# Kernel optimization log

Measured on AMD Instinct MI355X. Metric: run time of the kernel, lower is better.

Reference implementation:

```python
import jax, jax.numpy as jnp
import numpy as np

EPS = 1e-5

def _conv(x, w, groups=1):
    # x: NCHW, w: OIHW, VALID padding, stride 1
    return jax.lax.conv_general_dilated(
        x, w, window_strides=(1, 1), padding='VALID',
        feature_group_count=groups,
        dimension_numbers=('NCHW', 'OIHW', 'NCHW'))

def _bn(x, gamma, beta, mean, var):
    # eval-mode BatchNorm2d over channel dim
    inv = jax.lax.rsqrt(var + EPS) * gamma
    return x * inv[None, :, None, None] + (beta - mean * inv)[None, :, None, None]

def _xcorr_depthwise(x, kernel):
    # per-sample depthwise cross-correlation via grouped conv
    B, C, H, W = x.shape
    xr = x.reshape(1, B * C, H, W)
    kr = kernel.reshape(B * C, 1, kernel.shape[2], kernel.shape[3])
    out = _conv(xr, kr, groups=B * C)  # [1, B*C, Ho, Wo]
    return out.reshape(B, C, out.shape[2], out.shape[3])

def setup_inputs() -> dict:
    key = jax.random.key(0)
    ks = jax.random.split(key, 16)
    B, Cin, H, Oc = 128, 256, 256, 256
    inp = {
        'kernel': jax.random.normal(ks[0], (B, Cin, 7, 7), jnp.float32),
        'search': jax.random.normal(ks[1], (B, Cin, 31, 31), jnp.float32),
        # conv_kernel tower
        'wk': jax.random.normal(ks[2], (H, Cin, 3, 3), jnp.float32) * 0.05,
        'gk': jax.random.normal(ks[3], (H,), jnp.float32) * 0.1 + 1.0,
        'bk': jax.random.normal(ks[4], (H,), jnp.float32) * 0.1,
        'mk': jax.random.normal(ks[5], (H,), jnp.float32) * 0.1,
        'vk': jax.random.uniform(ks[6], (H,), jnp.float32) + 0.5,
        # conv_search tower
        'ws': jax.random.normal(ks[7], (H, Cin, 3, 3), jnp.float32) * 0.05,
        'gs': jax.random.normal(ks[8], (H,), jnp.float32) * 0.1 + 1.0,
        'bs': jax.random.normal(ks[9], (H,), jnp.float32) * 0.1,
        'ms': jax.random.normal(ks[10], (H,), jnp.float32) * 0.1,
        'vs': jax.random.uniform(ks[11], (H,), jnp.float32) + 0.5,
        # head: 1x1 conv -> BN -> ReLU -> 1x1 conv (with bias)
        'wh1': jax.random.normal(ks[12], (H, H, 1, 1), jnp.float32) * 0.05,
        'gh': jax.random.normal(ks[13], (H,), jnp.float32) * 0.1 + 1.0,
        'bh': jax.random.normal(ks[14], (H,), jnp.float32) * 0.1,
        'mh': jnp.zeros((H,), jnp.float32),
        'vh': jnp.ones((H,), jnp.float32),
        'wh2': jax.random.normal(ks[15], (Oc, H, 1, 1), jnp.float32) * 0.05,
        'bh2': jnp.zeros((Oc,), jnp.float32),
    }
    return inp

def reference(kernel, search, wk, gk, bk, mk, vk, ws, gs, bs, ms, vs,
              wh1, gh, bh, mh, vh, wh2, bh2):
    k = jax.nn.relu(_bn(_conv(kernel, wk), gk, bk, mk, vk))   # [B,H,5,5]
    s = jax.nn.relu(_bn(_conv(search, ws), gs, bs, ms, vs))   # [B,H,29,29]
    feat = _xcorr_depthwise(s, k)                              # [B,H,25,25]
    h = jax.nn.relu(_bn(_conv(feat, wh1), gh, bh, mh, vh))
    out = _conv(h, wh2) + bh2[None, :, None, None]            # [B,Oc,25,25]
    return out
```

## Files before the change

### kernel.cpp

```cpp
#include <hip/hip_runtime.h>
#include <hip/hip_bf16.h>
#include <cstdint>
#include <cstddef>

typedef unsigned short u16;
typedef __attribute__((ext_vector_type(8))) __bf16 bf16x8;
typedef __attribute__((ext_vector_type(4))) float f32x4;

#define EPS_BN 1e-5f

__device__ __forceinline__ u16 f2bf(float f) {
    union { float f; uint32_t u; } v; v.f = f;
    uint32_t u = v.u;
    u += 0x7FFFu + ((u >> 16) & 1u);
    return (u16)(u >> 16);
}
__device__ __forceinline__ float bf2f(u16 s) {
    union { uint32_t u; float f; } v; v.u = ((uint32_t)s) << 16;
    return v.f;
}

union Pack8 { u16 u[8]; uint4 v4; };
union Pack4 { u16 u[4]; uint2 v2; };

typedef __attribute__((address_space(1))) const unsigned char as1c;
typedef __attribute__((address_space(3))) unsigned char as3;
__device__ __forceinline__ void gld_lds16(const void* g, void* l) {
    __builtin_amdgcn_global_load_lds((as1c*)g, (as3*)l, 16, 0, 0);
}

__device__ __forceinline__ void tr_tile(const float* __restrict__ in,
                                        u16* __restrict__ out,
                                        int P, int b, int p0)
{
    const int w  = threadIdx.x >> 6;
    const int ln = threadIdx.x & 63;
    const int p  = p0 + ln;
    const bool ok = (p < P);
    const int pc = ok ? p : (P - 1);
    const float* ib = in + ((size_t)b * 256 + w * 64) * P + pc;

    float v[64];
    #pragma unroll
    for (int i = 0; i < 64; i++)
        v[i] = ib[(size_t)i * P];

    if (ok) {
        u16* ob = out + ((size_t)(b * P + p)) * 256 + w * 64;
        #pragma unroll
        for (int k = 0; k < 8; k++) {
            Pack8 pk;
            #pragma unroll
            for (int i = 0; i < 8; i++)
                pk.u[i] = f2bf(v[k * 8 + i]);
            *(uint4*)(ob + k * 8) = pk.v4;
        }
    }
}

__global__ __launch_bounds__(256)
void tr_all(const float* __restrict__ s, const float* __restrict__ k,
            u16* __restrict__ so, u16* __restrict__ ko)
{
    int blk = blockIdx.x;
    if (blk < 2048) {
        tr_tile(s, so, 961, blk >> 4, (blk & 15) * 64);
    } else {
        tr_tile(k, ko, 49, blk - 2048, 0);
    }
}

template<int TAPS, bool NHWC_OUT, typename OutT, bool RELU>
__global__ __launch_bounds__(256)
void conv_gemm(const u16* __restrict__ in, const u16* __restrict__ W,
               const float* __restrict__ scale, const float* __restrict__ shift,
               OutT* __restrict__ out, int Hi, int Wi, int Ho, int Wo)
{
    constexpr int KT = TAPS * 256;
    constexpr int KB = KT / 64;
    const int HoWo = Ho * Wo;

    __shared__ u16 Alds[8192];
    __shared__ u16 Blds[8192];

    const int tid = threadIdx.x;
    const int it = blockIdx.x;
    const int jt = blockIdx.y;
    const int wv = tid >> 6;
    const int lane = tid & 63;

    const int c8 = tid & 7;
    const int t3 = tid >> 3;
    const int csw = c8 ^ (t3 & 7);

    const u16* gA[4];
    const u16* gB[4];
    #pragma unroll
    for (int q = 0; q < 4; q++) {
        int r = q * 32 + t3;
        gA[q] = W + (size_t)(it * 128 + r) * KT + csw * 8;
        int jg = jt * 128 + r;
        int bb = jg / HoWo;
        int msp = jg - bb * HoWo;
        int oyp = msp / Wo;
        int oxp = msp - oyp * Wo;
        gB[q] = in + ((size_t)(bb * Hi + oyp) * Wi + oxp) * 256 + csw * 8;
    }

    const int wi = (wv >> 1) * 64;
    const int wj = (wv & 1) * 64;
    const int lr = lane & 15;
    const int lq = lane >> 4;

    f32x4 acc[4][4];
    #pragma unroll
    for (int a = 0; a < 4; a++)
        #pragma unroll
        for (int b = 0; b < 4; b++)
            acc[a][b] = (f32x4){0.f, 0.f, 0.f, 0.f};

    for (int kb = 0; kb < KB; kb++) {
        const int tap = (TAPS == 1) ? 0 : (kb >> 2);
        const int c0  = (TAPS == 1) ? (kb * 64) : ((kb & 3) * 64);
        int ky = 0, kx = 0;
        if (TAPS == 9) { ky = tap / 3; kx = tap - ky * 3; }
        const int aoff = tap * 256 + c0;
        const int boff = (ky * Wi + kx) * 256 + c0;
        __syncthreads();
        #pragma unroll
        for (int q = 0; q < 4; q++)
            gld_lds16(gA[q] + aoff, Alds + q * 2048 + wv * 512);
        #pragma unroll
        for (int q = 0; q < 4; q++)
            gld_lds16(gB[q] + boff, Blds + q * 2048 + wv * 512);
        __syncthreads();
        #pragma unroll
        for (int ks = 0; ks < 2; ks++) {
            bf16x8 af[4], bfr[4];
            const int ck = ks * 4 + lq;
            #pragma unroll
            for (int f = 0; f < 4; f++) {
                int ra = wi + f * 16 + lr;
                af[f]  = *(const bf16x8*)&Alds[ra * 64 + ((ck ^ (ra & 7)) * 8)];
                int rb = wj + f * 16 + lr;
                bfr[f] = *(const bf16x8*)&Blds[rb * 64 + ((ck ^ (rb & 7)) * 8)];
            }
            #pragma unroll
            for (int fi = 0; fi < 4; fi++)
                #pragma unroll
                for (int fj = 0; fj < 4; fj++)
                    acc[fi][fj] = __builtin_amdgcn_mfma_f32_16x16x32_bf16(
                        af[fi], bfr[fj], acc[fi][fj], 0, 0, 0);
        }
    }

    if constexpr (NHWC_OUT) {
        int jc[4];
        #pragma unroll
        for (int fj = 0; fj < 4; fj++) jc[fj] = jt * 128 + wj + fj * 16 + lr;
        #pragma unroll
        for (int fi = 0; fi < 4; fi++) {
            int rb = it * 128 + wi + fi * 16 + lq * 4;
            f32x4 sc = *(const f32x4*)&scale[rb];
            f32x4 sh = *(const f32x4*)&shift[rb];
            #pragma unroll
            for (int fj = 0; fj < 4; fj++) {
                Pack4 pk;
                #pragma unroll
                for (int reg = 0; reg < 4; reg++) {
                    float v = acc[fi][fj][reg] * sc[reg] + sh[reg];
                    if (RELU) v = fmaxf(v, 0.f);
                    pk.u[reg] = f2bf(v);
                }
                *(uint2*)&((u16*)out)[(size_t)jc[fj] * 256 + rb] = pk.v2;
            }
        }
    } else {
        int jcb[4], jcm[4];
        #pragma unroll
        for (int fj = 0; fj < 4; fj++) {
            int jc = jt * 128 + wj + fj * 16 + lr;
            int b = jc / HoWo;
            jcb[fj] = b; jcm[fj] = jc - b * HoWo;
        }
        #pragma unroll
        for (int fi = 0; fi < 4; fi++) {
            int rb = it * 128 + wi + fi * 16 + lq * 4;
            f32x4 sc = *(const f32x4*)&scale[rb];
            f32x4 sh = *(const f32x4*)&shift[rb];
            #pragma unroll
            for (int reg = 0; reg < 4; reg++) {
                int r = rb + reg;
                #pragma unroll
                for (int fj = 0; fj < 4; fj++) {
                    float v = acc[fi][fj][reg] * sc[reg] + sh[reg];
                    if (RELU) v = fmaxf(v, 0.f);
                    size_t o = ((size_t)(jcb[fj] * 256 + r)) * HoWo + jcm[fj];
                    ((float*)out)[o] = v;
                }
            }
        }
    }
}

template<int TAPS>
__global__ __launch_bounds__(512, 2)
void conv_gemm8(const u16* __restrict__ in, const u16* __restrict__ W,
                const float* __restrict__ scale, const float* __restrict__ shift,
                u16* __restrict__ out, int Hi, int Wi, int Ho, int Wo, int npix)
{
    constexpr int KT = TAPS * 256;
    constexpr int NT = KT / 64;
    static_assert(NT >= 2, "pipeline needs >=2 K-tiles");
    const int HoWo = Ho * Wo;

    __shared__ u16 ldsbuf[65536];

    const int tid  = threadIdx.x;
    const int jt0  = blockIdx.x;
    const int nwg  = gridDim.x;
    const int q8   = nwg >> 3, r8 = nwg & 7;
    const int xcd  = jt0 & 7, sidx = jt0 >> 3;
    const int jt   = (xcd < r8 ? xcd * (q8 + 1)
                               : r8 * (q8 + 1) + (xcd - r8) * q8) + sidx;
    const int wv   = tid >> 6;
    const int lane = tid & 63;
    const int wm   = wv >> 2;
    const int wn   = wv & 3;
    const int lr   = lane & 15;
    const int lq   = lane >> 4;

    const int c8  = tid & 7;
    const int rr  = tid >> 3;
    const int csw = (c8 ^ (rr & 7)) * 8;

    const u16* gA00 = W + (size_t)(rr)        * KT + csw;
    const u16* gA01 = W + (size_t)(64  + rr)  * KT + csw;
    const u16* gA10 = W + (size_t)(128 + rr)  * KT + csw;
    const u16* gA11 = W + (size_t)(192 + rr)  * KT + csw;

    const u16* gB00; const u16* gB01; const u16* gB10; const u16* gB11;
    {
        #pragma unroll
        for (int hq = 0; hq < 4; hq++) {
            int jg = jt * 256 + hq * 64 + rr;
            if (jg >= npix) jg = npix - 1;
            int bb  = jg / HoWo;
            int msp = jg - bb * HoWo;
            int oy  = msp / Wo;
            int ox  = msp - oy * Wo;
            const u16* p = in + ((size_t)((bb * Hi + oy) * Wi + ox)) * 256 + csw;
            if (hq == 0) gB00 = p; else if (hq == 1) gB01 = p;
            else if (hq == 2) gB10 = p; else gB11 = p;
        }
    }

    #define STA(slot_, h_, j_) do { if ((j_) < NT) {                          \
        const int _ao = (j_) * 64;                                            \
        u16* _d = ldsbuf + (slot_) * 32768 + (h_) * 8192 + wv * 512;          \
        gld_lds16(((h_) ? gA10 : gA00) + _ao, _d);                            \
        gld_lds16(((h_) ? gA11 : gA01) + _ao, _d + 4096);                     \
    } } while (0)

    #define STB(slot_, h_, j_) do { if ((j_) < NT) {                          \
        int _ky = 0, _kx = 0;                                                 \
        if (TAPS == 9) { int _t = (j_) >> 2; _ky = _t / 3; _kx = _t - _ky*3; }\
        const int _bo = (_ky * Wi + _kx) * 256 + ((j_) & 3) * 64;             \
        u16* _d = ldsbuf + (slot_) * 32768 + 16384 + (h_) * 8192 + wv * 512;  \
        gld_lds16(((h_) ? gB10 : gB00) + _bo, _d);                            \
        gld_lds16(((h_) ? gB11 : gB01) + _bo, _d + 4096);                     \
    } } while (0)

    #define DSA(RQ) do {                                                      \
        _Pragma("unroll")                                                     \
        for (int ks = 0; ks < 2; ks++) {                                      \
            const int _cx = ks ? x1 : x0;                                     \
            _Pragma("unroll")                                                 \
            for (int f = 0; f < 4; f++) {                                     \
                int _ra = wm * 128 + (RQ) * 64 + f * 16 + lr;                 \
                aF[ks][f] = *(const bf16x8*)&ldsbuf[sA + _ra * 64 + _cx];     \
            }                                                                 \
        }                                                                     \
    } while (0)

    #define DSB(BF, CQ) do {                                                  \
        _Pragma("unroll")                                                     \
        for (int ks = 0; ks < 2; ks++) {                                      \
            const int _cx = ks ? x1 : x0;                                     \
            _Pragma("unroll")                                                 \
            for (int g = 0; g < 2; g++) {                                     \
                int _rb = wn * 64 + (CQ) * 32 + g * 16 + lr;                  \
                BF[ks][g] = *(const bf16x8*)&ldsbuf[sB + _rb * 64 + _cx];     \
            }                                                                 \
        }                                                                     \
    } while (0)

    #define MFMA16(AF, BF, RO, CO) do {                                       \
        __builtin_amdgcn_s_setprio(1);                                        \
        _Pragma("unroll")                                                     \
        for (int ks = 0; ks < 2; ks++)                                        \
            _Pragma("unroll")                                                 \
            for (int f = 0; f < 4; f++)                                       \
                _Pragma("unroll")                                             \
                for (int g = 0; g < 2; g++)                                   \
                    acc[(RO) + f][(CO) + g] =                                 \
                        __builtin_amdgcn_mfma_f32_16x16x32_bf16(              \
                            AF[ks][f], BF[ks][g], acc[(RO) + f][(CO) + g],    \
                            0, 0, 0);                                         \
        __builtin_amdgcn_s_setprio(0);                                        \
    } while (0)

    f32x4 acc[8][4];
    #pragma unroll
    for (int a = 0; a < 8; a++)
        #pragma unroll
        for (int b = 0; b < 4; b++)
            acc[a][b] = (f32x4){0.f, 0.f, 0.f, 0.f};

    const int x0 = ((0 * 4 + lq) ^ (lr & 7)) * 8;
    const int x1 = ((1 * 4 + lq) ^ (lr & 7)) * 8;

    STA(0, 0, 0); STA(0, 1, 0); STB(0, 0, 0); STB(0, 1, 0);
    STB(1, 0, 1); STA(1, 0, 1);
    asm volatile("s_waitcnt vmcnt(4)" ::: "memory");
    __builtin_amdgcn_s_barrier();

    for (int j = 0; j < NT; j++) {
        const int slot = j & 1;
        const int nsl  = slot ^ 1;
        const int sA   = slot * 32768;
        const int sB   = sA + 16384;
        bf16x8 aF[2][4], bF0[2][2], bF1[2][2];

        DSA(0); DSB(bF0, 0);
        STA(nsl, 1, j + 1);
        __builtin_amdgcn_s_barrier();
        asm volatile("s_waitcnt lgkmcnt(0)" ::: "memory");
        MFMA16(aF, bF0, 0, 0);
        __builtin_amdgcn_s_barrier();

        DSB(bF1, 1);
        STB(nsl, 1, j + 1);
        __builtin_amdgcn_s_barrier();
        asm volatile("s_waitcnt lgkmcnt(0)" ::: "memory");
        MFMA16(aF, bF1, 0, 2);
        __builtin_amdgcn_s_barrier();

        DSA(1);
        STB(slot, 0, j + 2);
        __builtin_amdgcn_s_barrier();
        asm volatile("s_waitcnt lgkmcnt(0)" ::: "memory");
        MFMA16(aF, bF0, 4, 0);
        __builtin_amdgcn_s_barrier();

        STA(slot, 0, j + 2);
        if (j + 2 < NT) asm volatile("s_waitcnt vmcnt(4)" ::: "memory");
        else            asm volatile("s_waitcnt vmcnt(0)" ::: "memory");
        __builtin_amdgcn_s_barrier();
        MFMA16(aF, bF1, 4, 2);
        __builtin_amdgcn_s_barrier();
    }

    #undef STA
    #undef STB
    #undef DSA
    #undef DSB
    #undef MFMA16

    const int obase = jt * 256;
    #pragma unroll
    for (int fr = 0; fr < 8; fr++) {
        const int rb = wm * 128 + fr * 16 + lq * 4;
        const f32x4 sc = *(const f32x4*)&scale[rb];
        const f32x4 sh = *(const f32x4*)&shift[rb];
        #pragma unroll
        for (int fc = 0; fc < 4; fc++) {
            const int jc = obase + wn * 64 + fc * 16 + lr;
            if (jc < npix) {
                Pack4 pk;
                #pragma unroll
                for (int reg = 0; reg < 4; reg++) {
                    float v = acc[fr][fc][reg] * sc[reg] + sh[reg];
                    v = fmaxf(v, 0.f);
                    pk.u[reg] = f2bf(v);
                }
                *(uint2*)&out[(size_t)jc * 256 + rb] = pk.v2;
            }
        }
    }
}

__global__ __launch_bounds__(256)
void xcorr_kernel(const u16* __restrict__ s, const u16* __restrict__ k,
                  u16* __restrict__ out)
{
    const int b = blockIdx.x / 25;
    const int oy = blockIdx.x - b * 25;
    const int c = threadIdx.x;

    float kf[25];
    #pragma unroll
    for (int t = 0; t < 25; t++)
        kf[t] = bf2f(k[((size_t)(b * 25 + t)) * 256 + c]);

    float acc[25];
    #pragma unroll
    for (int i = 0; i < 25; i++) acc[i] = 0.f;

    for (int dy = 0; dy < 5; dy++) {
        float row[29];
        const u16* sp = s + ((size_t)(b * 29 + oy + dy) * 29) * 256 + c;
        #pragma unroll
        for (int x = 0; x < 29; x++) row[x] = bf2f(sp[(size_t)x * 256]);
        #pragma unroll
        for (int dx = 0; dx < 5; dx++) {
            float kv = kf[dy * 5 + dx];
            #pragma unroll
            for (int ox = 0; ox < 25; ox++)
                acc[ox] += row[ox + dx] * kv;
        }
    }
    u16* op = out + ((size_t)(b * 25 + oy) * 25) * 256 + c;
    #pragma unroll
    for (int ox = 0; ox < 25; ox++)
        op[(size_t)ox * 256] = f2bf(acc[ox]);
}

__global__ __launch_bounds__(256)
void prep_all(const float* __restrict__ wk, const float* __restrict__ wsw,
              const float* __restrict__ wh1, const float* __restrict__ wh2,
              const float* gk, const float* bk, const float* mk, const float* vk,
              const float* gs, const float* bs, const float* ms, const float* vs,
              const float* gh, const float* bh, const float* mh, const float* vh,
              const float* bh2,
              u16* __restrict__ Wk2, u16* __restrict__ Ws2,
              u16* __restrict__ Wh1b, u16* __restrict__ Wh2b,
              float* sk, float* tk, float* ss, float* ts,
              float* sh, float* th, float* s5, float* t5)
{
    int blk = blockIdx.x;
    int tidx = threadIdx.x;
    if (blk < 4608) {
        const float* w = (blk < 2304) ? wk : wsw;
        u16* o = (blk < 2304) ? Wk2 : Ws2;
        int idx = (blk % 2304) * 256 + tidx;
        int oc = idx / 2304, rem = idx - oc * 2304;
        int tap = rem >> 8, c = rem & 255;
        o[idx] = f2bf(w[oc * 2304 + c * 9 + tap]);
    } else if (blk < 5120) {
        const float* w = (blk < 4864) ? wh1 : wh2;
        u16* o = (blk < 4864) ? Wh1b : Wh2b;
        int idx = ((blk - 4608) % 256) * 256 + tidx;
        o[idx] = f2bf(w[idx]);
    } else {
        int i = tidx;
        float iv;
        iv = rsqrtf(vk[i] + EPS_BN) * gk[i]; sk[i] = iv; tk[i] = bk[i] - mk[i] * iv;
        iv = rsqrtf(vs[i] + EPS_BN) * gs[i]; ss[i] = iv; ts[i] = bs[i] - ms[i] * iv;
        iv = rsqrtf(vh[i] + EPS_BN) * gh[i]; sh[i] = iv; th[i] = bh[i] - mh[i] * iv;
        s5[i] = 1.f; t5[i] = bh2[i];
    }
}

extern "C" void kernel_launch(void* const* d_in, const int* in_sizes, int n_in,
                              void* d_out, int out_size, void* d_ws, size_t ws_size,
                              hipStream_t stream)
{
    const float* in_kernel = (const float*)d_in[0];
    const float* in_search = (const float*)d_in[1];
    const float* wk  = (const float*)d_in[2];
    const float* gk  = (const float*)d_in[3];
    const float* bk  = (const float*)d_in[4];
    const float* mk  = (const float*)d_in[5];
    const float* vk  = (const float*)d_in[6];
    const float* wsw = (const float*)d_in[7];
    const float* gs  = (const float*)d_in[8];
    const float* bs  = (const float*)d_in[9];
    const float* ms  = (const float*)d_in[10];
    const float* vs  = (const float*)d_in[11];
    const float* wh1 = (const float*)d_in[12];
    const float* gh  = (const float*)d_in[13];
    const float* bh  = (const float*)d_in[14];
    const float* mh  = (const float*)d_in[15];
    const float* vh  = (const float*)d_in[16];
    const float* wh2 = (const float*)d_in[17];
    const float* bh2 = (const float*)d_in[18];
    float* out = (float*)d_out;

    char* w = (char*)d_ws;
    u16* Wk2 = (u16*)w;  w += 1179648;
    u16* Ws2 = (u16*)w;  w += 1179648;
    u16* Wh1 = (u16*)w;  w += 131072;
    u16* Wh2 = (u16*)w;  w += 131072;
    float* sk = (float*)w; w += 1024;
    float* tk = (float*)w; w += 1024;
    float* ss = (float*)w; w += 1024;
    float* ts = (float*)w; w += 1024;
    float* sh = (float*)w; w += 1024;
    float* th = (float*)w; w += 1024;
    float* s5 = (float*)w; w += 1024;
    float* t5 = (float*)w; w += 1024;
    u16* kfeat = (u16*)w; w += 1638400;
    u16* sfeat = (u16*)w; w += 55115776;
    u16* feat  = (u16*)w; w += 40960000;
    u16* ktr   = (u16*)w; w += 3211264;
    u16* strA  = (u16*)w; w += 62980096;
    u16* hbuf  = strA;

    tr_all<<<2048 + 128, 256, 0, stream>>>(in_search, in_kernel, strA, ktr);
    prep_all<<<5121, 256, 0, stream>>>(wk, wsw, wh1, wh2,
                                       gk, bk, mk, vk, gs, bs, ms, vs,
                                       gh, bh, mh, vh, bh2,
                                       Wk2, Ws2, Wh1, Wh2,
                                       sk, tk, ss, ts, sh, th, s5, t5);

    conv_gemm<9, true, u16, true><<<dim3(2, 25), 256, 0, stream>>>(
        ktr, Wk2, sk, tk, kfeat, 7, 7, 5, 5);
    conv_gemm8<9><<<dim3(421), 512, 0, stream>>>(
        strA, Ws2, ss, ts, sfeat, 31, 31, 29, 29, 128 * 841);
    xcorr_kernel<<<128 * 25, 256, 0, stream>>>(sfeat, kfeat, feat);
    conv_gemm<1, true, u16, true><<<dim3(2, 625), 256, 0, stream>>>(
        feat, Wh1, sh, th, hbuf, 25, 25, 25, 25);
    conv_gemm<1, false, float, false><<<dim3(2, 625), 256, 0, stream>>>(
        hbuf, Wh2, s5, t5, out, 25, 25, 25, 25);

    (void)in_sizes; (void)n_in; (void)out_size; (void)ws_size;
}
```

Baseline: 549.7 us.

## Restructure search conv GEMM to 4 waves, coalesce transpose via LDS, batch xcorr rows

The main search-tower conv GEMM drops from 8 waves to 4 waves with 256 threads. Each wave now computes a 128x128 tile with a 8x8 accumulator array, and the LDS/MFMA pipeline is reordered with finer lgkmcnt waits and fewer barriers. The input transpose kernel now stages through a swizzled LDS tile so the bf16 NHWC stores are fully coalesced. The depthwise xcorr kernel computes 5 output rows per block and reuses each loaded search row across them, cutting redundant global loads at the cost of more registers (125 accumulators) and fewer blocks.

```diff
diff --git a/kernel.cpp b/kernel.cpp
--- a/kernel.cpp
+++ b/kernel.cpp
@@ -33,27 +33,36 @@
                                         u16* __restrict__ out,
                                         int P, int b, int p0)
 {
-    const int w  = threadIdx.x >> 6;
-    const int ln = threadIdx.x & 63;
-    const int p  = p0 + ln;
-    const bool ok = (p < P);
-    const int pc = ok ? p : (P - 1);
-    const float* ib = in + ((size_t)b * 256 + w * 64) * P + pc;
-
-    float v[64];
-    #pragma unroll
-    for (int i = 0; i < 64; i++)
-        v[i] = ib[(size_t)i * P];
-
-    if (ok) {
-        u16* ob = out + ((size_t)(b * P + p)) * 256 + w * 64;
+    __shared__ u16 t_lds[64 * 256];
+    const int tid = threadIdx.x;
+    const int w  = tid >> 6;
+    const int ln = tid & 63;
+
+    {
+        const int p  = p0 + ln;
+        const int pc = (p < P) ? p : (P - 1);
+        const float* ib = in + ((size_t)b * 256 + w * 64) * P + pc;
         #pragma unroll
         for (int k = 0; k < 8; k++) {
             Pack8 pk;
             #pragma unroll
             for (int i = 0; i < 8; i++)
-                pk.u[i] = f2bf(v[k * 8 + i]);
-            *(uint4*)(ob + k * 8) = pk.v4;
+                pk.u[i] = f2bf(ib[(size_t)(k * 8 + i) * P]);
+            const int chunk = w * 8 + k;
+            *(uint4*)&t_lds[ln * 256 + ((chunk ^ (ln & 31)) * 8)] = pk.v4;
+        }
+    }
+    __syncthreads();
+    {
+        const int ch = tid & 31;
+        const int pg = tid >> 5;
+        #pragma unroll
+        for (int it = 0; it < 8; it++) {
+            int px = it * 8 + pg;
+            int p  = p0 + px;
+            uint4 v = *(const uint4*)&t_lds[px * 256 + ((ch ^ (px & 31)) * 8)];
+            if (p < P)
+                *(uint4*)(out + ((size_t)(b * P + p)) * 256 + ch * 8) = v;
         }
     }
 }
@@ -204,8 +213,8 @@
 }
 
 template<int TAPS>
-__global__ __launch_bounds__(512, 2)
-void conv_gemm8(const u16* __restrict__ in, const u16* __restrict__ W,
+__global__ __launch_bounds__(256, 1)
+void conv_gemm4(const u16* __restrict__ in, const u16* __restrict__ W,
                 const float* __restrict__ scale, const float* __restrict__ shift,
                 u16* __restrict__ out, int Hi, int Wi, int Ho, int Wo, int npix)
 {
@@ -223,10 +232,11 @@
     const int xcd  = jt0 & 7, sidx = jt0 >> 3;
     const int jt   = (xcd < r8 ? xcd * (q8 + 1)
                                : r8 * (q8 + 1) + (xcd - r8) * q8) + sidx;
+
     const int wv   = tid >> 6;
     const int lane = tid & 63;
-    const int wm   = wv >> 2;
-    const int wn   = wv & 3;
+    const int wm   = wv >> 1;
+    const int wn   = wv & 1;
     const int lr   = lane & 15;
     const int lq   = lane >> 4;
 
@@ -234,32 +244,27 @@
     const int rr  = tid >> 3;
     const int csw = (c8 ^ (rr & 7)) * 8;
 
-    const u16* gA00 = W + (size_t)(rr)        * KT + csw;
-    const u16* gA01 = W + (size_t)(64  + rr)  * KT + csw;
-    const u16* gA10 = W + (size_t)(128 + rr)  * KT + csw;
-    const u16* gA11 = W + (size_t)(192 + rr)  * KT + csw;
-
-    const u16* gB00; const u16* gB01; const u16* gB10; const u16* gB11;
-    {
-        #pragma unroll
-        for (int hq = 0; hq < 4; hq++) {
-            int jg = jt * 256 + hq * 64 + rr;
-            if (jg >= npix) jg = npix - 1;
-            int bb  = jg / HoWo;
-            int msp = jg - bb * HoWo;
-            int oy  = msp / Wo;
-            int ox  = msp - oy * Wo;
-            const u16* p = in + ((size_t)((bb * Hi + oy) * Wi + ox)) * 256 + csw;
-            if (hq == 0) gB00 = p; else if (hq == 1) gB01 = p;
-            else if (hq == 2) gB10 = p; else gB11 = p;
-        }
+    const u16* gA0 = W + (size_t)rr * KT + csw;
+
+    const u16* gB[8];
+    #pragma unroll
+    for (int hq = 0; hq < 8; hq++) {
+        int jg = jt * 256 + hq * 32 + rr;
+        if (jg >= npix) jg = npix - 1;
+        int bb  = jg / HoWo;
+        int msp = jg - bb * HoWo;
+        int oy  = msp / Wo;
+        int ox  = msp - oy * Wo;
+        gB[hq] = in + ((size_t)((bb * Hi + oy) * Wi + ox)) * 256 + csw;
     }
 
     #define STA(slot_, h_, j_) do { if ((j_) < NT) {                          \
-        const int _ao = (j_) * 64;                                            \
+        const size_t _ao = (size_t)(j_) * 64;                                 \
         u16* _d = ldsbuf + (slot_) * 32768 + (h_) * 8192 + wv * 512;          \
-        gld_lds16(((h_) ? gA10 : gA00) + _ao, _d);                            \
-        gld_lds16(((h_) ? gA11 : gA01) + _ao, _d + 4096);                     \
+        gld_lds16(gA0 + (size_t)((h_) * 128 +  0) * KT + _ao, _d);            \
+        gld_lds16(gA0 + (size_t)((h_) * 128 + 32) * KT + _ao, _d + 2048);     \
+        gld_lds16(gA0 + (size_t)((h_) * 128 + 64) * KT + _ao, _d + 4096);     \
+        gld_lds16(gA0 + (size_t)((h_) * 128 + 96) * KT + _ao, _d + 6144);     \
     } } while (0)
 
     #define STB(slot_, h_, j_) do { if ((j_) < NT) {                          \
@@ -267,42 +272,44 @@
         if (TAPS == 9) { int _t = (j_) >> 2; _ky = _t / 3; _kx = _t - _ky*3; }\
         const int _bo = (_ky * Wi + _kx) * 256 + ((j_) & 3) * 64;             \
         u16* _d = ldsbuf + (slot_) * 32768 + 16384 + (h_) * 8192 + wv * 512;  \
-        gld_lds16(((h_) ? gB10 : gB00) + _bo, _d);                            \
-        gld_lds16(((h_) ? gB11 : gB01) + _bo, _d + 4096);                     \
+        gld_lds16(gB[(h_) * 4 + 0] + _bo, _d);                                \
+        gld_lds16(gB[(h_) * 4 + 1] + _bo, _d + 2048);                         \
+        gld_lds16(gB[(h_) * 4 + 2] + _bo, _d + 4096);                         \
+        gld_lds16(gB[(h_) * 4 + 3] + _bo, _d + 6144);                         \
     } } while (0)
 
-    #define DSA(RQ) do {                                                      \
+    #define DSA(DST, RQ) do {                                                 \
         _Pragma("unroll")                                                     \
         for (int ks = 0; ks < 2; ks++) {                                      \
             const int _cx = ks ? x1 : x0;                                     \
             _Pragma("unroll")                                                 \
             for (int f = 0; f < 4; f++) {                                     \
                 int _ra = wm * 128 + (RQ) * 64 + f * 16 + lr;                 \
-                aF[ks][f] = *(const bf16x8*)&ldsbuf[sA + _ra * 64 + _cx];     \
+                DST[ks][f] = *(const bf16x8*)&ldsbuf[sA + _ra * 64 + _cx];    \
             }                                                                 \
         }                                                                     \
     } while (0)
 
-    #define DSB(BF, CQ) do {                                                  \
+    #define DSB(DST, CQ) do {                                                 \
         _Pragma("unroll")                                                     \
         for (int ks = 0; ks < 2; ks++) {                                      \
             const int _cx = ks ? x1 : x0;                                     \
             _Pragma("unroll")                                                 \
-            for (int g = 0; g < 2; g++) {                                     \
-                int _rb = wn * 64 + (CQ) * 32 + g * 16 + lr;                  \
-                BF[ks][g] = *(const bf16x8*)&ldsbuf[sB + _rb * 64 + _cx];     \
+            for (int g = 0; g < 4; g++) {                                     \
+                int _rb = wn * 128 + (CQ) * 64 + g * 16 + lr;                 \
+                DST[ks][g] = *(const bf16x8*)&ldsbuf[sB + _rb * 64 + _cx];    \
             }                                                                 \
         }                                                                     \
     } while (0)
 
-    #define MFMA16(AF, BF, RO, CO) do {                                       \
+    #define MFMA32(AF, BF, RO, CO) do {                                       \
         __builtin_amdgcn_s_setprio(1);                                        \
         _Pragma("unroll")                                                     \
         for (int ks = 0; ks < 2; ks++)                                        \
             _Pragma("unroll")                                                 \
             for (int f = 0; f < 4; f++)                                       \
                 _Pragma("unroll")                                             \
-                for (int g = 0; g < 2; g++)                                   \
+                for (int g = 0; g < 4; g++)                                   \
                     acc[(RO) + f][(CO) + g] =                                 \
                         __builtin_amdgcn_mfma_f32_16x16x32_bf16(              \
                             AF[ks][f], BF[ks][g], acc[(RO) + f][(CO) + g],    \
@@ -310,19 +317,19 @@
         __builtin_amdgcn_s_setprio(0);                                        \
     } while (0)
 
-    f32x4 acc[8][4];
+    f32x4 acc[8][8];
     #pragma unroll
     for (int a = 0; a < 8; a++)
         #pragma unroll
-        for (int b = 0; b < 4; b++)
+        for (int b = 0; b < 8; b++)
             acc[a][b] = (f32x4){0.f, 0.f, 0.f, 0.f};
 
     const int x0 = ((0 * 4 + lq) ^ (lr & 7)) * 8;
     const int x1 = ((1 * 4 + lq) ^ (lr & 7)) * 8;
 
-    STA(0, 0, 0); STA(0, 1, 0); STB(0, 0, 0); STB(0, 1, 0);
+    STA(0, 0, 0); STB(0, 0, 0); STA(0, 1, 0); STB(0, 1, 0);
     STB(1, 0, 1); STA(1, 0, 1);
-    asm volatile("s_waitcnt vmcnt(4)" ::: "memory");
+    asm volatile("s_waitcnt vmcnt(8)" ::: "memory");
     __builtin_amdgcn_s_barrier();
 
     for (int j = 0; j < NT; j++) {
@@ -330,34 +337,31 @@
         const int nsl  = slot ^ 1;
         const int sA   = slot * 32768;
         const int sB   = sA + 16384;
-        bf16x8 aF[2][4], bF0[2][2], bF1[2][2];
-
-        DSA(0); DSB(bF0, 0);
+        bf16x8 aF[2][4], aG[2][4], bF0[2][4], bF1[2][4];
+
+        DSA(aF, 0); DSB(bF0, 0); DSB(bF1, 1); DSA(aG, 1);
         STA(nsl, 1, j + 1);
+        STB(nsl, 1, j + 1);
+
+        asm volatile("s_waitcnt lgkmcnt(15)" ::: "memory");
+        __builtin_amdgcn_sched_barrier(0);
+        MFMA32(aF, bF0, 0, 0);
+
+        asm volatile("s_waitcnt lgkmcnt(8)" ::: "memory");
+        __builtin_amdgcn_sched_barrier(0);
+        MFMA32(aF, bF1, 0, 4);
         __builtin_amdgcn_s_barrier();
+
+        STB(slot, 0, j + 2);
         asm volatile("s_waitcnt lgkmcnt(0)" ::: "memory");
-        MFMA16(aF, bF0, 0, 0);
+        __builtin_amdgcn_sched_barrier(0);
+        MFMA32(aG, bF0, 4, 0);
         __builtin_amdgcn_s_barrier();
 
-        DSB(bF1, 1);
-        STB(nsl, 1, j + 1);
-        __builtin_amdgcn_s_barrier();
-        asm volatile("s_waitcnt lgkmcnt(0)" ::: "memory");
-        MFMA16(aF, bF1, 0, 2);
-        __builtin_amdgcn_s_barrier();
-
-        DSA(1);
-        STB(slot, 0, j + 2);
-        __builtin_amdgcn_s_barrier();
-        asm volatile("s_waitcnt lgkmcnt(0)" ::: "memory");
-        MFMA16(aF, bF0, 4, 0);
-        __builtin_amdgcn_s_barrier();
-
         STA(slot, 0, j + 2);
-        if (j + 2 < NT) asm volatile("s_waitcnt vmcnt(4)" ::: "memory");
+        MFMA32(aG, bF1, 4, 4);
+        if (j + 2 < NT) asm volatile("s_waitcnt vmcnt(8)" ::: "memory");
         else            asm volatile("s_waitcnt vmcnt(0)" ::: "memory");
-        __builtin_amdgcn_s_barrier();
-        MFMA16(aF, bF1, 4, 2);
         __builtin_amdgcn_s_barrier();
     }
 
@@ -365,7 +369,7 @@
     #undef STB
     #undef DSA
     #undef DSB
-    #undef MFMA16
+    #undef MFMA32
 
     const int obase = jt * 256;
     #pragma unroll
@@ -374,8 +378,8 @@
         const f32x4 sc = *(const f32x4*)&scale[rb];
         const f32x4 sh = *(const f32x4*)&shift[rb];
         #pragma unroll
-        for (int fc = 0; fc < 4; fc++) {
-            const int jc = obase + wn * 64 + fc * 16 + lr;
+        for (int fc = 0; fc < 8; fc++) {
+            const int jc = obase + wn * 128 + fc * 16 + lr;
             if (jc < npix) {
                 Pack4 pk;
                 #pragma unroll
@@ -394,36 +398,48 @@
 void xcorr_kernel(const u16* __restrict__ s, const u16* __restrict__ k,
                   u16* __restrict__ out)
 {
-    const int b = blockIdx.x / 25;
-    const int oy = blockIdx.x - b * 25;
-    const int c = threadIdx.x;
+    const int b  = blockIdx.x / 5;
+    const int og = blockIdx.x - b * 5;
+    const int c  = threadIdx.x;
 
     float kf[25];
     #pragma unroll
     for (int t = 0; t < 25; t++)
         kf[t] = bf2f(k[((size_t)(b * 25 + t)) * 256 + c]);
 
-    float acc[25];
-    #pragma unroll
-    for (int i = 0; i < 25; i++) acc[i] = 0.f;
-
-    for (int dy = 0; dy < 5; dy++) {
+    float acc[5][25];
+    #pragma unroll
+    for (int o = 0; o < 5; o++)
+        #pragma unroll
+        for (int i = 0; i < 25; i++) acc[o][i] = 0.f;
+
+    #pragma unroll
+    for (int r = 0; r < 9; r++) {
         float row[29];
-        const u16* sp = s + ((size_t)(b * 29 + oy + dy) * 29) * 256 + c;
+        const u16* sp = s + ((size_t)(b * 29 + og * 5 + r) * 29) * 256 + c;
         #pragma unroll
         for (int x = 0; x < 29; x++) row[x] = bf2f(sp[(size_t)x * 256]);
         #pragma unroll
-        for (int dx = 0; dx < 5; dx++) {
-            float kv = kf[dy * 5 + dx];
-            #pragma unroll
-            for (int ox = 0; ox < 25; ox++)
-                acc[ox] += row[ox + dx] * kv;
-        }
-    }
-    u16* op = out + ((size_t)(b * 25 + oy) * 25) * 256 + c;
-    #pragma unroll
-    for (int ox = 0; ox < 25; ox++)
-        op[(size_t)ox * 256] = f2bf(acc[ox]);
+        for (int dy = 0; dy < 5; dy++) {
+            const int o = r - dy;
+            if (o >= 0 && o < 5) {
+                #pragma unroll
+                for (int dx = 0; dx < 5; dx++) {
+                    float kv = kf[dy * 5 + dx];
+                    #pragma unroll
+                    for (int ox = 0; ox < 25; ox++)
+                        acc[o][ox] += row[ox + dx] * kv;
+                }
+            }
+        }
+    }
+    #pragma unroll
+    for (int o = 0; o < 5; o++) {
+        u16* op = out + ((size_t)(b * 25 + og * 5 + o) * 25) * 256 + c;
+        #pragma unroll
+        for (int ox = 0; ox < 25; ox++)
+            op[(size_t)ox * 256] = f2bf(acc[o][ox]);
+    }
 }
 
 __global__ __launch_bounds__(256)
@@ -516,9 +532,9 @@
 
     conv_gemm<9, true, u16, true><<<dim3(2, 25), 256, 0, stream>>>(
         ktr, Wk2, sk, tk, kfeat, 7, 7, 5, 5);
-    conv_gemm8<9><<<dim3(421), 512, 0, stream>>>(
+    conv_gemm4<9><<<dim3(421), 256, 0, stream>>>(
         strA, Ws2, ss, ts, sfeat, 31, 31, 29, 29, 128 * 841);
-    xcorr_kernel<<<128 * 25, 256, 0, stream>>>(sfeat, kfeat, feat);
+    xcorr_kernel<<<128 * 5, 256, 0, stream>>>(sfeat, kfeat, feat);
     conv_gemm<1, true, u16, true><<<dim3(2, 625), 256, 0, stream>>>(
         feat, Wh1, sh, th, hbuf, 25, 25, 25, 25);
     conv_gemm<1, false, float, false><<<dim3(2, 625), 256, 0, stream>>>(
```

After: 591.3 us. 1.08x slower.

## Fuse head 1x1 convs, reuse rows in xcorr, stage transpose via LDS

Applied to the files above, without the earlier changes.

Merges the two 1x1 head convolutions into one kernel that keeps the ReLU'd intermediate in LDS, so the hidden activation no longer round-trips through global memory. The depthwise xcorr now computes 5 output rows per block and reuses each loaded search row across them, cutting redundant global reads, though each thread now holds a 125-float accumulator and register pressure rises. The input transpose goes through a swizzled LDS tile so global stores are coalesced 16-byte writes. The fused head also uses fewer blocks (625), which may lower occupancy.

```diff
diff --git a/kernel.cpp b/kernel.cpp
--- a/kernel.cpp
+++ b/kernel.cpp
@@ -33,27 +33,36 @@
                                         u16* __restrict__ out,
                                         int P, int b, int p0)
 {
-    const int w  = threadIdx.x >> 6;
-    const int ln = threadIdx.x & 63;
-    const int p  = p0 + ln;
-    const bool ok = (p < P);
-    const int pc = ok ? p : (P - 1);
-    const float* ib = in + ((size_t)b * 256 + w * 64) * P + pc;
-
-    float v[64];
-    #pragma unroll
-    for (int i = 0; i < 64; i++)
-        v[i] = ib[(size_t)i * P];
-
-    if (ok) {
-        u16* ob = out + ((size_t)(b * P + p)) * 256 + w * 64;
+    __shared__ u16 t_lds[64 * 256];
+    const int tid = threadIdx.x;
+    const int w  = tid >> 6;
+    const int ln = tid & 63;
+
+    {
+        const int p  = p0 + ln;
+        const int pc = (p < P) ? p : (P - 1);
+        const float* ib = in + ((size_t)b * 256 + w * 64) * P + pc;
         #pragma unroll
         for (int k = 0; k < 8; k++) {
             Pack8 pk;
             #pragma unroll
             for (int i = 0; i < 8; i++)
-                pk.u[i] = f2bf(v[k * 8 + i]);
-            *(uint4*)(ob + k * 8) = pk.v4;
+                pk.u[i] = f2bf(ib[(size_t)(k * 8 + i) * P]);
+            const int chunk = w * 8 + k;
+            *(uint4*)&t_lds[ln * 256 + ((chunk ^ (ln & 31)) * 8)] = pk.v4;
+        }
+    }
+    __syncthreads();
+    {
+        const int ch = tid & 31;
+        const int pg = tid >> 5;
+        #pragma unroll
+        for (int it = 0; it < 8; it++) {
+            int px = it * 8 + pg;
+            int p  = p0 + px;
+            uint4 v = *(const uint4*)&t_lds[px * 256 + ((ch ^ (px & 31)) * 8)];
+            if (p < P)
+                *(uint4*)(out + ((size_t)(b * P + p)) * 256 + ch * 8) = v;
         }
     }
 }
@@ -390,40 +399,185 @@
     }
 }
 
+__global__ __launch_bounds__(512)
+void head_fused(const u16* __restrict__ feat, const u16* __restrict__ W1,
+                const u16* __restrict__ W2,
+                const float* __restrict__ scale1, const float* __restrict__ shift1,
+                const float* __restrict__ bias2,
+                float* __restrict__ out)
+{
+    __shared__ u16 Alds[16384];
+    __shared__ u16 Blds[8192];
+    __shared__ u16 Hlds[32768];
+
+    const int tid  = threadIdx.x;
+    const int jt   = blockIdx.x;
+    const int wv   = tid >> 6;
+    const int lane = tid & 63;
+    const int wm   = wv >> 2;
+    const int wn   = wv & 3;
+    const int lr   = lane & 15;
+    const int lq   = lane >> 4;
+
+    const int c8  = tid & 7;
+    const int rr  = tid >> 3;
+    const int csw = (c8 ^ (rr & 7)) * 8;
+
+    f32x4 acc[8][2];
+    #pragma unroll
+    for (int f = 0; f < 8; f++)
+        #pragma unroll
+        for (int g = 0; g < 2; g++)
+            acc[f][g] = (f32x4){0.f, 0.f, 0.f, 0.f};
+
+    for (int kb = 0; kb < 4; kb++) {
+        __syncthreads();
+        #pragma unroll
+        for (int q = 0; q < 4; q++)
+            gld_lds16(W1 + (size_t)(q * 64 + rr) * 256 + kb * 64 + csw,
+                      Alds + q * 4096 + wv * 512);
+        #pragma unroll
+        for (int q = 0; q < 2; q++)
+            gld_lds16(feat + (size_t)(jt * 128 + q * 64 + rr) * 256 + kb * 64 + csw,
+                      Blds + q * 4096 + wv * 512);
+        __syncthreads();
+        #pragma unroll
+        for (int ks = 0; ks < 2; ks++) {
+            const int ck = ks * 4 + lq;
+            bf16x8 af[8], bf[2];
+            #pragma unroll
+            for (int f = 0; f < 8; f++) {
+                int ra = wm * 128 + f * 16 + lr;
+                af[f] = *(const bf16x8*)&Alds[ra * 64 + ((ck ^ (ra & 7)) * 8)];
+            }
+            #pragma unroll
+            for (int g = 0; g < 2; g++) {
+                int rb = wn * 32 + g * 16 + lr;
+                bf[g] = *(const bf16x8*)&Blds[rb * 64 + ((ck ^ (rb & 7)) * 8)];
+            }
+            #pragma unroll
+            for (int f = 0; f < 8; f++)
+                #pragma unroll
+                for (int g = 0; g < 2; g++)
+                    acc[f][g] = __builtin_amdgcn_mfma_f32_16x16x32_bf16(
+                        af[f], bf[g], acc[f][g], 0, 0, 0);
+        }
+    }
+
+    #pragma unroll
+    for (int f = 0; f < 8; f++) {
+        const int rb = wm * 128 + f * 16 + lq * 4;
+        const f32x4 sc = *(const f32x4*)&scale1[rb];
+        const f32x4 sf = *(const f32x4*)&shift1[rb];
+        #pragma unroll
+        for (int g = 0; g < 2; g++) {
+            const int j = wn * 32 + g * 16 + lr;
+            Pack4 pk;
+            #pragma unroll
+            for (int r = 0; r < 4; r++) {
+                float v = acc[f][g][r] * sc[r] + sf[r];
+                v = fmaxf(v, 0.f);
+                pk.u[r] = f2bf(v);
+            }
+            const int ch = rb >> 3;
+            *(uint2*)&Hlds[j * 256 + ((ch ^ (j & 31)) * 8) + (rb & 7)] = pk.v2;
+            acc[f][g] = (f32x4){0.f, 0.f, 0.f, 0.f};
+        }
+    }
+
+    for (int kb = 0; kb < 4; kb++) {
+        __syncthreads();
+        #pragma unroll
+        for (int q = 0; q < 4; q++)
+            gld_lds16(W2 + (size_t)(q * 64 + rr) * 256 + kb * 64 + csw,
+                      Alds + q * 4096 + wv * 512);
+        __syncthreads();
+        #pragma unroll
+        for (int ks = 0; ks < 2; ks++) {
+            const int ck = ks * 4 + lq;
+            const int ch32 = kb * 8 + ck;
+            bf16x8 af[8], bf[2];
+            #pragma unroll
+            for (int f = 0; f < 8; f++) {
+                int ra = wm * 128 + f * 16 + lr;
+                af[f] = *(const bf16x8*)&Alds[ra * 64 + ((ck ^ (ra & 7)) * 8)];
+            }
+            #pragma unroll
+            for (int g = 0; g < 2; g++) {
+                int j = wn * 32 + g * 16 + lr;
+                bf[g] = *(const bf16x8*)&Hlds[j * 256 + ((ch32 ^ (j & 31)) * 8)];
+            }
+            #pragma unroll
+            for (int f = 0; f < 8; f++)
+                #pragma unroll
+                for (int g = 0; g < 2; g++)
+                    acc[f][g] = __builtin_amdgcn_mfma_f32_16x16x32_bf16(
+                        af[f], bf[g], acc[f][g], 0, 0, 0);
+        }
+    }
+
+    #pragma unroll
+    for (int f = 0; f < 8; f++) {
+        const int oc = wm * 128 + f * 16 + lq * 4;
+        const f32x4 b2 = *(const f32x4*)&bias2[oc];
+        #pragma unroll
+        for (int g = 0; g < 2; g++) {
+            const int j  = jt * 128 + wn * 32 + g * 16 + lr;
+            const int bb = j / 625;
+            const int pix = j - bb * 625;
+            #pragma unroll
+            for (int r = 0; r < 4; r++)
+                out[((size_t)(bb * 256 + oc + r)) * 625 + pix] = acc[f][g][r] + b2[r];
+        }
+    }
+}
+
 __global__ __launch_bounds__(256)
 void xcorr_kernel(const u16* __restrict__ s, const u16* __restrict__ k,
                   u16* __restrict__ out)
 {
-    const int b = blockIdx.x / 25;
-    const int oy = blockIdx.x - b * 25;
-    const int c = threadIdx.x;
+    const int b  = blockIdx.x / 5;
+    const int og = blockIdx.x - b * 5;
+    const int c  = threadIdx.x;
 
     float kf[25];
     #pragma unroll
     for (int t = 0; t < 25; t++)
         kf[t] = bf2f(k[((size_t)(b * 25 + t)) * 256 + c]);
 
-    float acc[25];
-    #pragma unroll
-    for (int i = 0; i < 25; i++) acc[i] = 0.f;
-
-    for (int dy = 0; dy < 5; dy++) {
+    float acc[5][25];
+    #pragma unroll
+    for (int o = 0; o < 5; o++)
+        #pragma unroll
+        for (int i = 0; i < 25; i++) acc[o][i] = 0.f;
+
+    #pragma unroll
+    for (int r = 0; r < 9; r++) {
         float row[29];
-        const u16* sp = s + ((size_t)(b * 29 + oy + dy) * 29) * 256 + c;
+        const u16* sp = s + ((size_t)(b * 29 + og * 5 + r) * 29) * 256 + c;
         #pragma unroll
         for (int x = 0; x < 29; x++) row[x] = bf2f(sp[(size_t)x * 256]);
         #pragma unroll
-        for (int dx = 0; dx < 5; dx++) {
-            float kv = kf[dy * 5 + dx];
-            #pragma unroll
-            for (int ox = 0; ox < 25; ox++)
-                acc[ox] += row[ox + dx] * kv;
-        }
-    }
-    u16* op = out + ((size_t)(b * 25 + oy) * 25) * 256 + c;
-    #pragma unroll
-    for (int ox = 0; ox < 25; ox++)
-        op[(size_t)ox * 256] = f2bf(acc[ox]);
+        for (int dy = 0; dy < 5; dy++) {
+            const int o = r - dy;
+            if (o >= 0 && o < 5) {
+                #pragma unroll
+                for (int dx = 0; dx < 5; dx++) {
+                    float kv = kf[dy * 5 + dx];
+                    #pragma unroll
+                    for (int ox = 0; ox < 25; ox++)
+                        acc[o][ox] += row[ox + dx] * kv;
+                }
+            }
+        }
+    }
+    #pragma unroll
+    for (int o = 0; o < 5; o++) {
+        u16* op = out + ((size_t)(b * 25 + og * 5 + o) * 25) * 256 + c;
+        #pragma unroll
+        for (int ox = 0; ox < 25; ox++)
+            op[(size_t)ox * 256] = f2bf(acc[o][ox]);
+    }
 }
 
 __global__ __launch_bounds__(256)
@@ -505,7 +659,6 @@
     u16* feat  = (u16*)w; w += 40960000;
     u16* ktr   = (u16*)w; w += 3211264;
     u16* strA  = (u16*)w; w += 62980096;
-    u16* hbuf  = strA;
 
     tr_all<<<2048 + 128, 256, 0, stream>>>(in_search, in_kernel, strA, ktr);
     prep_all<<<5121, 256, 0, stream>>>(wk, wsw, wh1, wh2,
@@ -518,11 +671,8 @@
         ktr, Wk2, sk, tk, kfeat, 7, 7, 5, 5);
     conv_gemm8<9><<<dim3(421), 512, 0, stream>>>(
         strA, Ws2, ss, ts, sfeat, 31, 31, 29, 29, 128 * 841);
-    xcorr_kernel<<<128 * 25, 256, 0, stream>>>(sfeat, kfeat, feat);
-    conv_gemm<1, true, u16, true><<<dim3(2, 625), 256, 0, stream>>>(
-        feat, Wh1, sh, th, hbuf, 25, 25, 25, 25);
-    conv_gemm<1, false, float, false><<<dim3(2, 625), 256, 0, stream>>>(
-        hbuf, Wh2, s5, t5, out, 25, 25, 25, 25);
+    xcorr_kernel<<<128 * 5, 256, 0, stream>>>(sfeat, kfeat, feat);
+    head_fused<<<625, 512, 0, stream>>>(feat, Wh1, Wh2, sh, th, t5, out);
 
     (void)in_sizes; (void)n_in; (void)out_size; (void)ws_size;
 }
```

After: 524.3 us. -4.6%, faster.
